# Performance work log

Hardware: AMD Instinct MI355X
Metric: run time of the kernel (lower is better)

Reference implementation:

```python
import jax, jax.numpy as jnp
import numpy as np

N_NODES = 100000
T = 1024        # number of visits / hyperedges (GRU sequence length)
IN = 128        # in_channel
HID = 256       # hid_channel


def setup_inputs() -> dict:
    key = jax.random.key(0)
    ks = jax.random.split(key, 7)
    X = jax.random.normal(ks[0], (N_NODES, IN), dtype=jnp.float32)
    H = jax.random.uniform(ks[1], (N_NODES, T), dtype=jnp.float32)
    s = 1.0 / np.sqrt(HID)  # torch default GRU init scale
    w_ih = jax.random.uniform(ks[2], (3 * HID, IN), jnp.float32, -s, s)
    w_hh = jax.random.uniform(ks[3], (3 * HID, HID), jnp.float32, -s, s)
    b_ih = jax.random.uniform(ks[4], (3 * HID,), jnp.float32, -s, s)
    b_hh = jax.random.uniform(ks[5], (3 * HID,), jnp.float32, -s, s)
    w_attn = jax.random.uniform(ks[6], (HID,), jnp.float32, -s, s)
    return {"X": X, "H": H, "w_ih": w_ih, "w_hh": w_hh,
            "b_ih": b_ih, "b_hh": b_hh, "w_attn": w_attn}


def _gru(visit_emb, w_ih, w_hh, b_ih, b_hh):
    # Precompute input-side gates for all timesteps: [T, 3H]
    gx = visit_emb @ w_ih.T + b_ih

    def step(h, gx_t):
        gh = h @ w_hh.T + b_hh
        xr, xz, xn = jnp.split(gx_t, 3)
        hr, hz, hn = jnp.split(gh, 3)
        r = jax.nn.sigmoid(xr + hr)
        z = jax.nn.sigmoid(xz + hz)
        n = jnp.tanh(xn + r * hn)
        h_new = (1.0 - z) * n + z * h
        return h_new, h_new

    h0 = jnp.zeros((HID,), visit_emb.dtype)
    _, hs = jax.lax.scan(step, h0, gx)
    return hs  # [T, HID]


def reference(X, H, w_ih, w_hh, b_ih, b_hh, w_attn):
    # visit_emb = H.T @ X : [T, IN]
    visit_emb = H.T @ X
    hs = _gru(visit_emb, w_ih, w_hh, b_ih, b_hh)          # [T, HID]
    alpha = jax.nn.softmax(hs @ w_attn)                    # [T]
    # sum(diag(alpha) @ hs, 0) == alpha-weighted sum of hidden states
    return alpha @ hs                                      # [HID]
```

## Files before the change

kernel.cpp:

```cpp
#include <hip/hip_runtime.h>
#include <hip/hip_fp16.h>

typedef _Float16 half8 __attribute__((ext_vector_type(8)));
typedef float f32x4 __attribute__((ext_vector_type(4)));

#define T_STEPS 1024
#define INC 128
#define HIDC 256
#define G3 768
#define NN 100000
#define KSPLIT 32
#define NCHUNK 3125
#define XS_STRIDE 144

__global__ __launch_bounds__(512) void k_phase1(const float* __restrict__ X,
                                                const float* __restrict__ Hm,
                                                float* __restrict__ part){
  const int bid = blockIdx.x;
  const int xcd = bid & 7;
  const int idx = bid >> 3;
  const int ks  = xcd * 4 + (idx & 3);
  const int tt  = idx >> 2;
  const int t0 = tt * 128;
  const int nbeg = ks * NCHUNK;
  const int nend = nbeg + NCHUNK;
  __shared__ float Hs[16][128];
  __shared__ float Xs[16 * XS_STRIDE];
  const int tid = threadIdx.x;
  const int tx = tid & 15;
  const int ty = tid >> 4;
  const int sr = tid >> 5;
  const int sc = tid & 31;
  const int xskew = tx * 8 + (tx >> 2) * 4;

  float acc[4][8];
  #pragma unroll
  for (int r = 0; r < 4; r++)
    #pragma unroll
    for (int q = 0; q < 8; q++) acc[r][q] = 0.f;

  float4 hv = make_float4(0.f,0.f,0.f,0.f), xv = make_float4(0.f,0.f,0.f,0.f);
  {
    int n = nbeg + sr;
    if (n < nend){
      hv = *(const float4*)(Hm + (size_t)n * T_STEPS + t0 + sc * 4);
      xv = *(const float4*)(X  + (size_t)n * INC + sc * 4);
    }
  }

  for (int n0 = nbeg; n0 < nend; n0 += 16){
    __builtin_amdgcn_s_barrier();
    asm volatile("" ::: "memory");
    *(float4*)&Hs[sr][sc * 4] = hv;
    {
      int g = sc >> 1, hf = sc & 1;
      *(float4*)&Xs[sr * XS_STRIDE + g * 8 + (g >> 2) * 4 + hf * 4] = xv;
    }
    asm volatile("s_waitcnt lgkmcnt(0)" ::: "memory");
    __builtin_amdgcn_s_barrier();
    asm volatile("" ::: "memory");

    {
      int nn = n0 + 16 + sr;
      hv = make_float4(0.f,0.f,0.f,0.f);
      xv = make_float4(0.f,0.f,0.f,0.f);
      if (nn < nend){
        hv = *(const float4*)(Hm + (size_t)nn * T_STEPS + t0 + sc * 4);
        xv = *(const float4*)(X  + (size_t)nn * INC + sc * 4);
      }
    }

    #pragma unroll
    for (int i = 0; i < 16; i++){
      float4 h4 = *(const float4*)&Hs[i][ty * 4];
      float4 x0 = *(const float4*)&Xs[i * XS_STRIDE + xskew];
      float4 x1 = *(const float4*)&Xs[i * XS_STRIDE + xskew + 4];
      float xr[8] = {x0.x,x0.y,x0.z,x0.w,x1.x,x1.y,x1.z,x1.w};
      float hr[4] = {h4.x,h4.y,h4.z,h4.w};
      #pragma unroll
      for (int r = 0; r < 4; r++)
        #pragma unroll
        for (int q = 0; q < 8; q++)
          acc[r][q] += hr[r] * xr[q];
    }
  }
  #pragma unroll
  for (int r = 0; r < 4; r++){
    size_t o = ((size_t)ks * T_STEPS + t0 + ty * 4 + r) * INC + tx * 8;
    *(float4*)&part[o]     = make_float4(acc[r][0], acc[r][1], acc[r][2], acc[r][3]);
    *(float4*)&part[o + 4] = make_float4(acc[r][4], acc[r][5], acc[r][6], acc[r][7]);
  }
}

__global__ __launch_bounds__(256) void k_reduce(const float* __restrict__ part,
                                                float* __restrict__ ve){
  int idx = blockIdx.x * 256 + threadIdx.x;
  float s = 0.f;
  #pragma unroll
  for (int ks = 0; ks < KSPLIT; ks++) s += part[(size_t)ks * (T_STEPS * INC) + idx];
  ve[idx] = s;
}

__global__ __launch_bounds__(768) void k_gx(const float* __restrict__ ve,
                                            const float* __restrict__ w_ih,
                                            const float* __restrict__ b_ih,
                                            const float* __restrict__ b_hh,
                                            float* __restrict__ gxq){
  const int t = blockIdx.x;
  const int j = threadIdx.x;
  __shared__ float4 v4[32];
  if (j < 32) v4[j] = *(const float4*)(ve + (size_t)t * INC + j * 4);
  __syncthreads();
  const float4* wr = (const float4*)(w_ih + (size_t)j * INC);
  float a0 = 0.f, a1 = 0.f, a2 = 0.f, a3 = 0.f;
  #pragma unroll
  for (int q = 0; q < 32; q++){
    float4 w = wr[q]; float4 v = v4[q];
    a0 += w.x * v.x; a1 += w.y * v.y; a2 += w.z * v.z; a3 += w.w * v.w;
  }
  float bias = b_ih[j] + (j < 512 ? b_hh[j] : 0.f);
  gxq[(size_t)t * 1024 + (j & 255) * 4 + (j >> 8)] = (a0 + a1) + (a2 + a3) + bias;
}

__global__ __launch_bounds__(1024) void k_gru(const float* __restrict__ w_hh,
                                              const float* __restrict__ b_hh,
                                              const float* __restrict__ gxq,
                                              float* __restrict__ hs){
  const int tid  = threadIdx.x;
  const int w    = tid >> 6;
  const int l    = tid & 63;
  const int col  = l & 15;
  const int quad = l >> 4;
  const int unit = w * 16 + col;

  __shared__ _Float16 hbuf[2][256];

  half8 Bf[3][8];
  #pragma unroll
  for (int g = 0; g < 3; g++){
    const float* wr = w_hh + (size_t)(g * 256 + unit) * HIDC + quad * 8;
    #pragma unroll
    for (int c = 0; c < 8; c++){
      float4 v0 = *(const float4*)(wr + c * 32);
      float4 v1 = *(const float4*)(wr + c * 32 + 4);
      half8 b;
      b[0]=(_Float16)v0.x; b[1]=(_Float16)v0.y; b[2]=(_Float16)v0.z; b[3]=(_Float16)v0.w;
      b[4]=(_Float16)v1.x; b[5]=(_Float16)v1.y; b[6]=(_Float16)v1.z; b[7]=(_Float16)v1.w;
      Bf[g][c] = b;
    }
  }
  const float bn = b_hh[512 + unit];
  float hprev = 0.f;
  if (tid < 256) hbuf[0][tid] = (_Float16)0.f;
  __syncthreads();

  f32x4 gq = *(const f32x4*)(gxq + (size_t)unit * 4);

  for (int t = 0; t < T_STEPS; t++){
    f32x4 dr = {0.f,0.f,0.f,0.f}, dz = {0.f,0.f,0.f,0.f}, dn = {0.f,0.f,0.f,0.f};
    const _Float16* hb = hbuf[t & 1];
    #pragma unroll
    for (int c = 0; c < 8; c++){
      half8 a = *(const half8*)(hb + c * 32 + quad * 8);
      dr = __builtin_amdgcn_mfma_f32_16x16x32_f16(a, Bf[0][c], dr, 0, 0, 0);
      dz = __builtin_amdgcn_mfma_f32_16x16x32_f16(a, Bf[1][c], dz, 0, 0, 0);
      dn = __builtin_amdgcn_mfma_f32_16x16x32_f16(a, Bf[2][c], dn, 0, 0, 0);
    }
    f32x4 gq_n = *(const f32x4*)(gxq + (size_t)(t + 1) * 1024 + unit * 4);

    float r = 1.f / (1.f + __expf(-(gq[0] + dr[0])));
    float z = 1.f / (1.f + __expf(-(gq[1] + dz[0])));
    float pre = gq[2] + r * (dn[0] + bn);
    float ax = fabsf(pre);
    float e = __expf(-2.f * ax);
    float th = (1.f - e) / (1.f + e);
    float n = copysignf(th, pre);
    float hnew = n + z * (hprev - n);
    hprev = hnew;
    if (quad == 0){
      hbuf[(t + 1) & 1][unit] = (_Float16)hnew;
      hs[(size_t)t * HIDC + unit] = hnew;
    }
    asm volatile("s_waitcnt lgkmcnt(0)" ::: "memory");
    __builtin_amdgcn_s_barrier();
    asm volatile("" ::: "memory");
    gq = gq_n;
  }
}

__global__ __launch_bounds__(64) void k_logits(const float* __restrict__ hs,
                                               const float* __restrict__ w_attn,
                                               float* __restrict__ logits){
  int t = blockIdx.x;
  int l = threadIdx.x;
  float4 hv = *(const float4*)(hs + (size_t)t * HIDC + l * 4);
  float4 wv = *(const float4*)(w_attn + l * 4);
  float p = hv.x * wv.x + hv.y * wv.y + hv.z * wv.z + hv.w * wv.w;
  #pragma unroll
  for (int o = 32; o > 0; o >>= 1) p += __shfl_down(p, o);
  if (l == 0) logits[t] = p;
}

__global__ __launch_bounds__(1024) void k_attn(const float* __restrict__ logits,
                                               const float* __restrict__ hs,
                                               float* __restrict__ out){
  __shared__ float sm[1024];
  __shared__ float al[1024];
  __shared__ float ps[4][HIDC];
  int tid = threadIdx.x;
  float lg = logits[tid];
  sm[tid] = lg; __syncthreads();
  for (int s = 512; s > 0; s >>= 1){
    if (tid < s) sm[tid] = fmaxf(sm[tid], sm[tid + s]);
    __syncthreads();
  }
  float mx = sm[0]; __syncthreads();
  float e = __expf(lg - mx);
  sm[tid] = e; __syncthreads();
  for (int s = 512; s > 0; s >>= 1){
    if (tid < s) sm[tid] += sm[tid + s];
    __syncthreads();
  }
  float inv = 1.f / sm[0];
  al[tid] = e * inv;
  __syncthreads();
  int c = tid & 255; int tq = tid >> 8;
  float acc = 0.f;
  for (int t = tq; t < T_STEPS; t += 4) acc += al[t] * hs[(size_t)t * HIDC + c];
  ps[tq][c] = acc; __syncthreads();
  if (tid < HIDC) out[tid] = (ps[0][tid] + ps[1][tid]) + (ps[2][tid] + ps[3][tid]);
}

extern "C" void kernel_launch(void* const* d_in, const int* in_sizes, int n_in,
                              void* d_out, int out_size, void* d_ws, size_t ws_size,
                              hipStream_t stream){
  const float* X      = (const float*)d_in[0];
  const float* Hm     = (const float*)d_in[1];
  const float* w_ih   = (const float*)d_in[2];
  const float* w_hh   = (const float*)d_in[3];
  const float* b_ih   = (const float*)d_in[4];
  const float* b_hh   = (const float*)d_in[5];
  const float* w_attn = (const float*)d_in[6];
  float* out = (float*)d_out;

  float* ws     = (float*)d_ws;
  float* part   = ws;
  float* ve     = part + 4194304;
  float* gxq    = ve + 131072;
  float* hs     = gxq + 1049600;
  float* logits = hs + 262144;

  k_phase1<<<256, 512, 0, stream>>>(X, Hm, part);
  k_reduce<<<512, 256, 0, stream>>>(part, ve);
  k_gx<<<1024, 768, 0, stream>>>(ve, w_ih, b_ih, b_hh, gxq);
  k_gru<<<1, 1024, 0, stream>>>(w_hh, b_hh, gxq, hs);
  k_logits<<<1024, 64, 0, stream>>>(hs, w_attn, logits);
  k_attn<<<1, 1024, 0, stream>>>(logits, hs, out);
}
```

Measured before the change: 2.317 ms.

## Replace MFMA GRU recurrence with per-thread fdot2 dot products

The sequential GRU kernel drops the 16x16x32 MFMA layout, in which only a quarter of lanes used their result, for 512 threads where each pair of threads splits one hidden unit's K dimension. Each thread holds 384 packed half2 weights in registers, accumulates with v_dot2 instructions, and the pair combines partials with a DPP lane swap. The aim is to cut wasted matrix work and shorten the per-step critical path of the 1024-step serial loop. The cost is heavy register pressure and more scalar instructions per thread, with a risk of spilling.

```diff
diff --git a/kernel.cpp b/kernel.cpp
--- a/kernel.cpp
+++ b/kernel.cpp
@@ -2,6 +2,7 @@
 #include <hip/hip_fp16.h>
 
 typedef _Float16 half8 __attribute__((ext_vector_type(8)));
+typedef _Float16 half2v __attribute__((ext_vector_type(2)));
 typedef float f32x4 __attribute__((ext_vector_type(4)));
 
 #define T_STEPS 1024
@@ -12,6 +13,11 @@
 #define KSPLIT 32
 #define NCHUNK 3125
 #define XS_STRIDE 144
+
+__device__ __forceinline__ float dpp_xor1(float v){
+  int t = __builtin_amdgcn_update_dpp(0, __float_as_int(v), 0xB1, 0xF, 0xF, true);
+  return __int_as_float(t);
+}
 
 __global__ __launch_bounds__(512) void k_phase1(const float* __restrict__ X,
                                                 const float* __restrict__ Hm,
@@ -122,31 +128,28 @@
   gxq[(size_t)t * 1024 + (j & 255) * 4 + (j >> 8)] = (a0 + a1) + (a2 + a3) + bias;
 }
 
-__global__ __launch_bounds__(1024) void k_gru(const float* __restrict__ w_hh,
-                                              const float* __restrict__ b_hh,
-                                              const float* __restrict__ gxq,
-                                              float* __restrict__ hs){
+__global__ __launch_bounds__(512, 2) void k_gru(const float* __restrict__ w_hh,
+                                                const float* __restrict__ b_hh,
+                                                const float* __restrict__ gxq,
+                                                float* __restrict__ hs){
   const int tid  = threadIdx.x;
-  const int w    = tid >> 6;
-  const int l    = tid & 63;
-  const int col  = l & 15;
-  const int quad = l >> 4;
-  const int unit = w * 16 + col;
+  const int unit = tid >> 1;
+  const int ks   = tid & 1;
+  const int k0   = ks * 128;
 
   __shared__ _Float16 hbuf[2][256];
 
-  half8 Bf[3][8];
+  half2v Bp[3][64];
   #pragma unroll
   for (int g = 0; g < 3; g++){
-    const float* wr = w_hh + (size_t)(g * 256 + unit) * HIDC + quad * 8;
-    #pragma unroll
-    for (int c = 0; c < 8; c++){
-      float4 v0 = *(const float4*)(wr + c * 32);
-      float4 v1 = *(const float4*)(wr + c * 32 + 4);
-      half8 b;
-      b[0]=(_Float16)v0.x; b[1]=(_Float16)v0.y; b[2]=(_Float16)v0.z; b[3]=(_Float16)v0.w;
-      b[4]=(_Float16)v1.x; b[5]=(_Float16)v1.y; b[6]=(_Float16)v1.z; b[7]=(_Float16)v1.w;
-      Bf[g][c] = b;
+    const float* wr = w_hh + (size_t)(g * 256 + unit) * HIDC + k0;
+    #pragma unroll
+    for (int c = 0; c < 32; c++){
+      float4 v = *(const float4*)(wr + c * 4);
+      half2v p0; p0[0] = (_Float16)v.x; p0[1] = (_Float16)v.y;
+      half2v p1; p1[0] = (_Float16)v.z; p1[1] = (_Float16)v.w;
+      Bp[g][2 * c]     = p0;
+      Bp[g][2 * c + 1] = p1;
     }
   }
   const float bn = b_hh[512 + unit];
@@ -157,34 +160,46 @@
   f32x4 gq = *(const f32x4*)(gxq + (size_t)unit * 4);
 
   for (int t = 0; t < T_STEPS; t++){
-    f32x4 dr = {0.f,0.f,0.f,0.f}, dz = {0.f,0.f,0.f,0.f}, dn = {0.f,0.f,0.f,0.f};
-    const _Float16* hb = hbuf[t & 1];
-    #pragma unroll
-    for (int c = 0; c < 8; c++){
-      half8 a = *(const half8*)(hb + c * 32 + quad * 8);
-      dr = __builtin_amdgcn_mfma_f32_16x16x32_f16(a, Bf[0][c], dr, 0, 0, 0);
-      dz = __builtin_amdgcn_mfma_f32_16x16x32_f16(a, Bf[1][c], dz, 0, 0, 0);
-      dn = __builtin_amdgcn_mfma_f32_16x16x32_f16(a, Bf[2][c], dn, 0, 0, 0);
+    const _Float16* hb = &hbuf[t & 1][k0];
+    float ar0 = 0.f, ar1 = 0.f, az0 = 0.f, az1 = 0.f, an0 = 0.f, an1 = 0.f;
+    #pragma unroll
+    for (int c = 0; c < 16; c++){
+      half8 hv = *(const half8*)(hb + c * 8);
+      #pragma unroll
+      for (int q = 0; q < 4; q++){
+        half2v hp; hp[0] = hv[2 * q]; hp[1] = hv[2 * q + 1];
+        if (c & 1){
+          ar1 = __builtin_amdgcn_fdot2(hp, Bp[0][4 * c + q], ar1, false);
+          az1 = __builtin_amdgcn_fdot2(hp, Bp[1][4 * c + q], az1, false);
+          an1 = __builtin_amdgcn_fdot2(hp, Bp[2][4 * c + q], an1, false);
+        } else {
+          ar0 = __builtin_amdgcn_fdot2(hp, Bp[0][4 * c + q], ar0, false);
+          az0 = __builtin_amdgcn_fdot2(hp, Bp[1][4 * c + q], az0, false);
+          an0 = __builtin_amdgcn_fdot2(hp, Bp[2][4 * c + q], an0, false);
+        }
+      }
     }
     f32x4 gq_n = *(const f32x4*)(gxq + (size_t)(t + 1) * 1024 + unit * 4);
 
-    float r = 1.f / (1.f + __expf(-(gq[0] + dr[0])));
-    float z = 1.f / (1.f + __expf(-(gq[1] + dz[0])));
-    float pre = gq[2] + r * (dn[0] + bn);
+    float dr = ar0 + ar1; dr += dpp_xor1(dr);
+    float dz = az0 + az1; dz += dpp_xor1(dz);
+    float dn = an0 + an1; dn += dpp_xor1(dn);
+
+    float r = 1.f / (1.f + __expf(-(gq[0] + dr)));
+    float z = 1.f / (1.f + __expf(-(gq[1] + dz)));
+    float pre = gq[2] + r * (dn + bn);
     float ax = fabsf(pre);
     float e = __expf(-2.f * ax);
     float th = (1.f - e) / (1.f + e);
     float n = copysignf(th, pre);
     float hnew = n + z * (hprev - n);
     hprev = hnew;
-    if (quad == 0){
+    if (ks == 0){
       hbuf[(t + 1) & 1][unit] = (_Float16)hnew;
       hs[(size_t)t * HIDC + unit] = hnew;
     }
-    asm volatile("s_waitcnt lgkmcnt(0)" ::: "memory");
-    __builtin_amdgcn_s_barrier();
-    asm volatile("" ::: "memory");
     gq = gq_n;
+    __syncthreads();
   }
 }
 
@@ -253,7 +268,7 @@
   k_phase1<<<256, 512, 0, stream>>>(X, Hm, part);
   k_reduce<<<512, 256, 0, stream>>>(part, ve);
   k_gx<<<1024, 768, 0, stream>>>(ve, w_ih, b_ih, b_hh, gxq);
-  k_gru<<<1, 1024, 0, stream>>>(w_hh, b_hh, gxq, hs);
+  k_gru<<<1, 512, 0, stream>>>(w_hh, b_hh, gxq, hs);
   k_logits<<<1024, 64, 0, stream>>>(hs, w_attn, logits);
   k_attn<<<1, 1024, 0, stream>>>(logits, hs, out);
 }
```

Measured after the change: 2.196 ms. 1.06x faster.
